# Optimization experiments

Hardware: AMD Instinct MI355X
Metric: run time of the kernel (lower is better)

The kernel has to match this reference:

```python
import jax, jax.numpy as jnp
import numpy as np

N = 100000      # number of nodes
FT = 256        # ft_in (hidden units)
NB_CLASSES = 16 # nb_classes
EPS = 1e-8      # torch.cosine_similarity eps


def setup_inputs() -> dict:
    key = jax.random.key(0)
    ks = jax.random.split(key, 7)
    seq = jax.random.normal(ks[0], (N, FT), dtype=jnp.float32)
    seq1 = jax.random.normal(ks[1], (N, FT), dtype=jnp.float32)
    labels = jax.random.randint(ks[2], (N,), 0, NB_CLASSES, dtype=jnp.int32)
    prompt1 = jax.random.normal(ks[3], (1, FT), dtype=jnp.float32)
    prompt2 = jax.random.normal(ks[4], (1, FT), dtype=jnp.float32)
    prompt3 = jax.random.normal(ks[5], (1, FT), dtype=jnp.float32)
    # weighted_prompt.reset_parameters: fixed init 0.5, 0.4, 0.3
    w_wp = jnp.array([[0.5, 0.4, 0.3]], dtype=jnp.float32)
    # weighted_feature.reset_parameters: fixed init 0.0, 1.0
    w_wf = jnp.array([[0.0, 1.0]], dtype=jnp.float32)
    # downstreamprompt.weight: xavier_uniform on [1, ft_in]
    bound = float(np.sqrt(6.0 / (1 + FT)))
    w_dp = jax.random.uniform(ks[6], (1, FT), jnp.float32, -bound, bound)
    a4 = jnp.array([0.1], dtype=jnp.float32)
    return {"seq": seq, "seq1": seq1, "labels": labels,
            "prompt1": prompt1, "prompt2": prompt2, "prompt3": prompt3,
            "w_wp": w_wp, "w_wf": w_wf, "w_dp": w_dp, "a4": a4}


def reference(seq, seq1, labels, prompt1, prompt2, prompt3, w_wp, w_wf, w_dp, a4):
    # weight = 1 + ELU(weighted_prompt(prompt))  -> [1, FT]
    prompt = jnp.concatenate([prompt1, prompt2, prompt3], axis=0)  # [3, FT]
    weight = 1.0 + jax.nn.elu(w_wp @ prompt)                       # [1, FT]
    rawret1 = weight * seq                                          # [N, FT]
    rawret2 = w_dp * seq                                            # downstreamprompt
    rawret3 = jax.nn.elu(w_wf[0, 0] * rawret1 + w_wf[0, 1] * rawret2)
    rawret = rawret3 + a4[0] * seq1                                 # [N, FT]
    # averageemb (train=1 path): per-class mean, zero-count classes stay 0
    sums = jax.ops.segment_sum(rawret, labels, num_segments=NB_CLASSES)  # [C, FT]
    counts = jax.ops.segment_sum(jnp.ones((rawret.shape[0],), rawret.dtype),
                                 labels, num_segments=NB_CLASSES)        # [C]
    ave = jnp.where(counts[:, None] > 0, sums / jnp.maximum(counts, 1.0)[:, None], sums)
    # fused per-pair cosine similarity: normalize + matmul (replaces N*C loop)
    num = rawret @ ave.T                                             # [N, C]
    denom = (jnp.linalg.norm(rawret, axis=1)[:, None] *
             jnp.linalg.norm(ave, axis=1)[None, :])
    ret = num / jnp.maximum(denom, EPS)
    return jax.nn.softmax(ret, axis=1)
```

## Files before the change

### kernel.cpp

```cpp
#include <hip/hip_runtime.h>
#include <hip/hip_bf16.h>

#define NROWS 100000
#define FT 256
#define NC 16
#define NBLK 512
#define NSL 8
#define SLICE (NBLK / NSL)

#define FPSCALE 1048576.0f
#define FPINV   (1.0f / 1048576.0f)

#define CW_AVEB 0
#define CW_NRM  2048
#define CW_PCNT 2064
#define CW_ST2C (CW_PCNT + NBLK*NC)
#define CW_ST2  (CW_ST2C + NSL*NC)
#define CW_PART (CW_ST2 + NSL*NC*FT)
#define CW_RAWB (CW_PART + NBLK*NC*FT)
#define CW_TOTAL (CW_RAWB + (NROWS*FT)/2)
#define CACHED_NEED_BYTES ((size_t)CW_TOTAL * 4)

#define WS_COEF 0
#define WS_SUMS 256
#define WS_CNTS 4352
#define WS_AVEB 4368
#define WS_NRM  6416

typedef float f32x4 __attribute__((ext_vector_type(4)));
typedef short bf16x8 __attribute__((ext_vector_type(8)));

static __device__ __forceinline__ float bfbits2f(unsigned int u16) {
    union { unsigned int i; float f; } v; v.i = u16 << 16; return v.f;
}
static __device__ __forceinline__ unsigned short f2bf(float f) {
    union { float f; unsigned int i; } v; v.f = f;
    unsigned int u = v.i;
    u += 0x7fffu + ((u >> 16) & 1u);
    return (unsigned short)(u >> 16);
}


__global__ __launch_bounds__(256) void k_accum_c(
    const float* __restrict__ seq,
    const float* __restrict__ seq1,
    const int* __restrict__ labels,
    const float* __restrict__ p1,
    const float* __restrict__ p2,
    const float* __restrict__ p3,
    const float* __restrict__ wwp,
    const float* __restrict__ wwf,
    const float* __restrict__ wdp,
    const float* __restrict__ a4p,
    float* __restrict__ ws)
{
    __shared__ __align__(16) float scoef[FT];
    __shared__ __align__(16) float lsumf[NC * FT];
    __shared__ int lcnti[4 * NC];
    const int tid = threadIdx.x;

    {
        float z = wwp[0] * p1[tid] + wwp[1] * p2[tid] + wwp[2] * p3[tid];
        float w = (z > 0.f) ? (1.f + z) : __expf(z);
        scoef[tid] = wwf[0] * w + wwf[1] * wdp[tid];
    }
    __syncthreads();

    const int wv = tid >> 6;
    const int l  = tid & 63;
    const int fl = l * 4;

    float cof[4];
    {
        const float4 c4 = *(const float4*)(scoef + fl);
        cof[0] = c4.x; cof[1] = c4.y; cof[2] = c4.z; cof[3] = c4.w;
    }
    const float a4v = a4p[0];
    unsigned int* rawb = (unsigned int*)(ws + CW_RAWB);

    float acc[NC][4];
#pragma unroll
    for (int c = 0; c < NC; ++c)
#pragma unroll
        for (int i = 0; i < 4; ++i) acc[c][i] = 0.f;
    int scnt[NC];
#pragma unroll
    for (int c = 0; c < NC; ++c) scnt[c] = 0;

    const int wg = blockIdx.x * 4 + wv;
    const int NQ = NROWS / 4;
    for (int q = wg; q < NQ; q += NBLK * 4) {
        const int r0 = q * 4;
        int lb[4]; float4 s4[4], t4[4];
#pragma unroll
        for (int j = 0; j < 4; ++j) {
            lb[j] = labels[r0 + j];
            s4[j] = *(const float4*)(seq  + (r0 + j) * FT + fl);
            t4[j] = *(const float4*)(seq1 + (r0 + j) * FT + fl);
        }
#pragma unroll
        for (int j = 0; j < 4; ++j) {
            const float ss[4] = {s4[j].x, s4[j].y, s4[j].z, s4[j].w};
            const float tt[4] = {t4[j].x, t4[j].y, t4[j].z, t4[j].w};
            float v[4];
#pragma unroll
            for (int i = 0; i < 4; ++i) {
                float u = cof[i] * ss[i];
                float r = (u > 0.f) ? u : (__expf(u) - 1.f);
                v[i] = r + a4v * tt[i];
            }
            uint2 pk;
            pk.x = (unsigned int)f2bf(v[0]) | ((unsigned int)f2bf(v[1]) << 16);
            pk.y = (unsigned int)f2bf(v[2]) | ((unsigned int)f2bf(v[3]) << 16);
            *(uint2*)(rawb + ((r0 + j) * FT + fl) / 2) = pk;
            const int ls = __builtin_amdgcn_readfirstlane(lb[j]);
#pragma unroll
            for (int c = 0; c < NC; ++c) {
                const float m = (ls == c) ? 1.0f : 0.0f;
#pragma unroll
                for (int i = 0; i < 4; ++i)
                    acc[c][i] = fmaf(m, v[i], acc[c][i]);
                scnt[c] += (ls == c) ? 1 : 0;
            }
        }
    }

    if (l == 0) {
#pragma unroll
        for (int c = 0; c < NC; ++c) lcnti[wv * NC + c] = scnt[c];
    }

    for (int w = 0; w < 4; ++w) {
        if (wv == w) {
#pragma unroll
            for (int c = 0; c < NC; ++c) {
                float4* p = (float4*)(lsumf + c * FT + fl);
                if (w == 0) {
                    float4 nv; nv.x = acc[c][0]; nv.y = acc[c][1];
                    nv.z = acc[c][2]; nv.w = acc[c][3];
                    *p = nv;
                } else {
                    float4 old = *p;
                    old.x += acc[c][0]; old.y += acc[c][1];
                    old.z += acc[c][2]; old.w += acc[c][3];
                    *p = old;
                }
            }
        }
        __syncthreads();
    }

    int* gpart = (int*)(ws + CW_PART) + blockIdx.x * (NC * FT);
    for (int idx = tid; idx < NC * FT; idx += 256)
        gpart[idx] = __float2int_rn(lsumf[idx] * FPSCALE);
    if (tid < NC) {
        int cc = lcnti[tid] + lcnti[NC + tid] + lcnti[2 * NC + tid]
               + lcnti[3 * NC + tid];
        ((int*)(ws + CW_PCNT))[blockIdx.x * NC + tid] = cc;
    }
}

__global__ __launch_bounds__(256) void k_reduce1(float* __restrict__ ws)
{
    const int c = blockIdx.x >> 3;
    const int r = blockIdx.x & 7;
    const int f = threadIdx.x;
    const int p0 = r * SLICE;
    const int* gpart = (const int*)(ws + CW_PART);
    int acc = 0;
#pragma unroll
    for (int p = 0; p < SLICE; ++p)
        acc += gpart[(p0 + p) * (NC * FT) + c * FT + f];
    ((int*)(ws + CW_ST2))[(r * NC + c) * FT + f] = acc;

    if (f < SLICE) {
        int cc = ((const int*)(ws + CW_PCNT))[(p0 + f) * NC + c];
#pragma unroll
        for (int o = 32; o > 0; o >>= 1) cc += __shfl_down(cc, o, 64);
        if (f == 0) ((int*)(ws + CW_ST2C))[r * NC + c] = cc;
    }
}

__global__ __launch_bounds__(256) void k_reduce2(float* __restrict__ ws)
{
    __shared__ float red[256];
    const int c = blockIdx.x;
    const int f = threadIdx.x;
    const int* st2  = (const int*)(ws + CW_ST2);
    const int* st2c = (const int*)(ws + CW_ST2C);
    long long isum = 0;
    int cnt = 0;
#pragma unroll
    for (int s = 0; s < NSL; ++s) {
        isum += (long long)st2[(s * NC + c) * FT + f];
        cnt  += st2c[s * NC + c];
    }
    float a = ((float)isum * FPINV) / fmaxf((float)cnt, 1.f);
    unsigned short ab = f2bf(a);
    ((unsigned short*)(ws + CW_AVEB))[c * FT + f] = ab;
    float af = bfbits2f(ab);

    red[f] = af * af;
    __syncthreads();
#pragma unroll
    for (int s = 128; s > 0; s >>= 1) {
        if (f < s) red[f] += red[f + s];
        __syncthreads();
    }
    if (f == 0) ws[CW_NRM + c] = sqrtf(red[0]);
}

__global__ __launch_bounds__(256) void k_out_c(
    const float* __restrict__ ws,
    float* __restrict__ out)
{
    const int tid = threadIdx.x;
    const int lane = tid & 63;
    const int wv   = tid >> 6;
    const int c = lane & 15;
    const int g = lane >> 4;

    const unsigned short* aveb = (const unsigned short*)(ws + CW_AVEB);
    const unsigned short* rawb = (const unsigned short*)(ws + CW_RAWB);
    bf16x8 bfrag[8];
#pragma unroll
    for (int kc = 0; kc < 8; ++kc)
        bfrag[kc] = *(const bf16x8*)(aveb + c * FT + kc * 32 + g * 8);
    const float na = ws[CW_NRM + c];

    const int ntiles = NROWS / 16;
    for (int tile = blockIdx.x * 4 + wv; tile < ntiles; tile += gridDim.x * 4) {
        const int rowbase = tile * 16;
        const int arow = rowbase + c;
        f32x4 accC = {0.f, 0.f, 0.f, 0.f};
        f32x4 accS = {0.f, 0.f, 0.f, 0.f};
#pragma unroll
        for (int kc = 0; kc < 8; ++kc) {
            bf16x8 afrag = *(const bf16x8*)(rawb + arow * FT + kc * 32 + g * 8);
            accC = __builtin_amdgcn_mfma_f32_16x16x32_bf16(afrag, bfrag[kc], accC, 0, 0, 0);
            accS = __builtin_amdgcn_mfma_f32_16x16x32_bf16(afrag, afrag,     accS, 0, 0, 0);
        }
#pragma unroll
        for (int q = 0; q < 4; ++q) {
            const float sd = __shfl(accS[q], g * 20 + q, 64);
            const float nr = sqrtf(fmaxf(sd, 0.f));
            const float denom = fmaxf(nr * na, 1e-8f);
            float cosv = accC[q] / denom;
            float mx = cosv;
#pragma unroll
            for (int o = 1; o < 16; o <<= 1) mx = fmaxf(mx, __shfl_xor(mx, o, 16));
            const float e = __expf(cosv - mx);
            float s = e;
#pragma unroll
            for (int o = 1; o < 16; o <<= 1) s += __shfl_xor(s, o, 16);
            out[(rowbase + g * 4 + q) * NC + c] = e / s;
        }
    }
}


__global__ void k_prep(const float* __restrict__ p1,
                       const float* __restrict__ p2,
                       const float* __restrict__ p3,
                       const float* __restrict__ wwp,
                       const float* __restrict__ wwf,
                       const float* __restrict__ wdp,
                       float* __restrict__ ws)
{
    int f = threadIdx.x;
    float z = wwp[0] * p1[f] + wwp[1] * p2[f] + wwp[2] * p3[f];
    float weight = (z > 0.f) ? (1.f + z) : __expf(z);
    ws[WS_COEF + f] = wwf[0] * weight + wwf[1] * wdp[f];
}

__global__ __launch_bounds__(1024) void k_accum(
    const float* __restrict__ seq,
    const float* __restrict__ seq1,
    const int* __restrict__ labels,
    const float* __restrict__ a4p,
    float* __restrict__ ws)
{
    __shared__ int lsum[NC * FT];
    __shared__ int lcnt[NC];
    const int tid = threadIdx.x;
    for (int i = tid; i < NC * FT; i += 1024) lsum[i] = 0;
    if (tid < NC) lcnt[tid] = 0;
    __syncthreads();

    const int rr = tid >> 5;
    const int m  = tid & 31;
    const int f0 = m * 8;
    const int mh = m >> 2;
    int off[8];
#pragma unroll
    for (int i = 0; i < 8; ++i) off[i] = (i + mh) & 7;

    float cof[8];
    {
        const float4 c0 = *(const float4*)(ws + WS_COEF + f0);
        const float4 c1 = *(const float4*)(ws + WS_COEF + f0 + 4);
        cof[0]=c0.x; cof[1]=c0.y; cof[2]=c0.z; cof[3]=c0.w;
        cof[4]=c1.x; cof[5]=c1.y; cof[6]=c1.z; cof[7]=c1.w;
    }
    const float a4v = a4p[0];

    for (int row = blockIdx.x * 32 + rr; row < NROWS; row += gridDim.x * 32) {
        const int lab = labels[row];
        const float4 sa  = *(const float4*)(seq  + row * FT + f0);
        const float4 sb  = *(const float4*)(seq  + row * FT + f0 + 4);
        const float4 ta  = *(const float4*)(seq1 + row * FT + f0);
        const float4 tb  = *(const float4*)(seq1 + row * FT + f0 + 4);
        const float s[8]  = {sa.x,sa.y,sa.z,sa.w, sb.x,sb.y,sb.z,sb.w};
        const float t[8]  = {ta.x,ta.y,ta.z,ta.w, tb.x,tb.y,tb.z,tb.w};
        int* base = lsum + lab * FT + f0;
#pragma unroll
        for (int i = 0; i < 8; ++i) {
            float u = cof[i] * s[i];
            float r = (u > 0.f) ? u : (__expf(u) - 1.f);
            atomicAdd(base + off[i], __float2int_rn((r + a4v * t[i]) * FPSCALE));
        }
        if (m == 0) atomicAdd(&lcnt[lab], 1);
    }
    __syncthreads();

    int* gsum = (int*)(ws + WS_SUMS);
    for (int idx = tid; idx < NC * FT; idx += 1024) {
        int p  = idx & 255;
        int mm = p >> 3;
        int r  = p & 7;
        int f  = (p & ~7) | ((r - (mm >> 2)) & 7);
        atomicAdd(gsum + (idx & ~255) + f, lsum[idx]);
    }
    if (tid < NC) atomicAdd((int*)(ws + WS_CNTS) + tid, lcnt[tid]);
}

__global__ void k_final(float* __restrict__ ws)
{
    __shared__ float nacc[NC];
    const int f = threadIdx.x;
    if (f < NC) nacc[f] = 0.f;
    __syncthreads();
    const int* gsum = (const int*)(ws + WS_SUMS);
    const int* gcnt = (const int*)(ws + WS_CNTS);
    unsigned short* aveb = (unsigned short*)(ws + WS_AVEB);
#pragma unroll
    for (int c = 0; c < NC; ++c) {
        float cnt = (float)gcnt[c];
        float a = ((float)gsum[c * FT + f] * FPINV) / fmaxf(cnt, 1.f);
        unsigned short ab = f2bf(a);
        aveb[c * FT + f] = ab;
        float af = bfbits2f(ab);
        atomicAdd(&nacc[c], af * af);
    }
    __syncthreads();
    if (f < NC) ws[WS_NRM + f] = sqrtf(nacc[f]);
}

__global__ __launch_bounds__(256) void k_out(
    const float* __restrict__ seq,
    const float* __restrict__ seq1,
    const float* __restrict__ a4p,
    const float* __restrict__ ws,
    float* __restrict__ out)
{
    __shared__ __align__(16) float scoef[FT];
    const int tid = threadIdx.x;
    for (int i = tid; i < FT; i += 256) scoef[i] = ws[WS_COEF + i];
    __syncthreads();

    const int lane = tid & 63;
    const int wv   = tid >> 6;
    const int c = lane & 15;
    const int g = lane >> 4;

    const unsigned short* aveb = (const unsigned short*)(ws + WS_AVEB);
    bf16x8 bfrag[8];
#pragma unroll
    for (int kc = 0; kc < 8; ++kc)
        bfrag[kc] = *(const bf16x8*)(aveb + c * FT + kc * 32 + g * 8);
    const float na  = ws[WS_NRM + c];
    const float a4v = a4p[0];

    const int ntiles = NROWS / 16;
    for (int tile = blockIdx.x * 4 + wv; tile < ntiles; tile += gridDim.x * 4) {
        const int rowbase = tile * 16;
        const int arow = rowbase + c;
        f32x4 accC = {0.f, 0.f, 0.f, 0.f};
        f32x4 accS = {0.f, 0.f, 0.f, 0.f};
#pragma unroll
        for (int kc = 0; kc < 8; ++kc) {
            const int k0 = kc * 32 + g * 8;
            const float4 sa = *(const float4*)(seq  + arow * FT + k0);
            const float4 sb = *(const float4*)(seq  + arow * FT + k0 + 4);
            const float4 ta = *(const float4*)(seq1 + arow * FT + k0);
            const float4 tb = *(const float4*)(seq1 + arow * FT + k0 + 4);
            const float4 c0 = *(const float4*)(scoef + k0);
            const float4 c1 = *(const float4*)(scoef + k0 + 4);
            const float s[8]  = {sa.x,sa.y,sa.z,sa.w, sb.x,sb.y,sb.z,sb.w};
            const float t[8]  = {ta.x,ta.y,ta.z,ta.w, tb.x,tb.y,tb.z,tb.w};
            const float cf[8] = {c0.x,c0.y,c0.z,c0.w, c1.x,c1.y,c1.z,c1.w};
            bf16x8 afrag;
#pragma unroll
            for (int i = 0; i < 8; ++i) {
                float u = cf[i] * s[i];
                float r = (u > 0.f) ? u : (__expf(u) - 1.f);
                afrag[i] = (short)f2bf(r + a4v * t[i]);
            }
            accC = __builtin_amdgcn_mfma_f32_16x16x32_bf16(afrag, bfrag[kc], accC, 0, 0, 0);
            accS = __builtin_amdgcn_mfma_f32_16x16x32_bf16(afrag, afrag,     accS, 0, 0, 0);
        }
#pragma unroll
        for (int q = 0; q < 4; ++q) {
            const float sd = __shfl(accS[q], g * 20 + q, 64);
            const float nr = sqrtf(fmaxf(sd, 0.f));
            const float denom = fmaxf(nr * na, 1e-8f);
            float cosv = accC[q] / denom;
            float mx = cosv;
#pragma unroll
            for (int o = 1; o < 16; o <<= 1) mx = fmaxf(mx, __shfl_xor(mx, o, 16));
            const float e = __expf(cosv - mx);
            float s = e;
#pragma unroll
            for (int o = 1; o < 16; o <<= 1) s += __shfl_xor(s, o, 16);
            out[(rowbase + g * 4 + q) * NC + c] = e / s;
        }
    }
}

extern "C" void kernel_launch(void* const* d_in, const int* in_sizes, int n_in,
                              void* d_out, int out_size, void* d_ws, size_t ws_size,
                              hipStream_t stream)
{
    const float* seq  = (const float*)d_in[0];
    const float* seq1 = (const float*)d_in[1];
    const int*   lab  = (const int*)d_in[2];
    const float* p1   = (const float*)d_in[3];
    const float* p2   = (const float*)d_in[4];
    const float* p3   = (const float*)d_in[5];
    const float* wwp  = (const float*)d_in[6];
    const float* wwf  = (const float*)d_in[7];
    const float* wdp  = (const float*)d_in[8];
    const float* a4   = (const float*)d_in[9];
    float* ws  = (float*)d_ws;
    float* out = (float*)d_out;

    if (ws_size >= CACHED_NEED_BYTES) {
        k_accum_c<<<NBLK,     256, 0, stream>>>(seq, seq1, lab, p1, p2, p3,
                                                wwp, wwf, wdp, a4, ws);
        k_reduce1<<<NC * NSL, 256, 0, stream>>>(ws);
        k_reduce2<<<NC,       256, 0, stream>>>(ws);
        k_out_c  <<<1568,     256, 0, stream>>>(ws, out);
    } else {
        hipMemsetAsync((char*)d_ws + WS_SUMS * sizeof(int), 0,
                       (NC * FT + NC) * sizeof(int), stream);
        k_prep <<<1,    256, 0, stream>>>(p1, p2, p3, wwp, wwf, wdp, ws);
        k_accum<<<512, 1024, 0, stream>>>(seq, seq1, lab, a4, ws);
        k_final<<<1,    256, 0, stream>>>(ws);
        k_out  <<<1568, 256, 0, stream>>>(seq, seq1, a4, ws, out);
    }
}
```

Measured before the change: 267.9 us.

## Widen accumulation kernel to 1024 threads with half-row wave split

```diff
diff --git a/kernel.cpp b/kernel.cpp
--- a/kernel.cpp
+++ b/kernel.cpp
@@ -41,7 +41,7 @@
 }
 
 
-__global__ __launch_bounds__(256) void k_accum_c(
+__global__ __launch_bounds__(1024, 8) void k_accum_c(
     const float* __restrict__ seq,
     const float* __restrict__ seq1,
     const int* __restrict__ labels,
@@ -56,10 +56,10 @@
 {
     __shared__ __align__(16) float scoef[FT];
     __shared__ __align__(16) float lsumf[NC * FT];
-    __shared__ int lcnti[4 * NC];
+    __shared__ int lcnti[16 * NC];
     const int tid = threadIdx.x;
 
-    {
+    if (tid < FT) {
         float z = wwp[0] * p1[tid] + wwp[1] * p2[tid] + wwp[2] * p3[tid];
         float w = (z > 0.f) ? (1.f + z) : __expf(z);
         scoef[tid] = wwf[0] * w + wwf[1] * wdp[tid];
@@ -68,82 +68,95 @@
 
     const int wv = tid >> 6;
     const int l  = tid & 63;
-    const int fl = l * 4;
-
-    float cof[4];
+    const int h  = wv & 1;
+    const int rbase = blockIdx.x * 8 + (wv >> 1);
+    const int fb = h * 128 + l * 2;
+
+    float2 cof2;
     {
-        const float4 c4 = *(const float4*)(scoef + fl);
-        cof[0] = c4.x; cof[1] = c4.y; cof[2] = c4.z; cof[3] = c4.w;
+        cof2 = *(const float2*)(scoef + fb);
     }
     const float a4v = a4p[0];
     unsigned int* rawb = (unsigned int*)(ws + CW_RAWB);
 
-    float acc[NC][4];
-#pragma unroll
-    for (int c = 0; c < NC; ++c)
-#pragma unroll
-        for (int i = 0; i < 4; ++i) acc[c][i] = 0.f;
-    int scnt[NC];
-#pragma unroll
-    for (int c = 0; c < NC; ++c) scnt[c] = 0;
-
-    const int wg = blockIdx.x * 4 + wv;
-    const int NQ = NROWS / 4;
-    for (int q = wg; q < NQ; q += NBLK * 4) {
-        const int r0 = q * 4;
-        int lb[4]; float4 s4[4], t4[4];
-#pragma unroll
-        for (int j = 0; j < 4; ++j) {
-            lb[j] = labels[r0 + j];
-            s4[j] = *(const float4*)(seq  + (r0 + j) * FT + fl);
-            t4[j] = *(const float4*)(seq1 + (r0 + j) * FT + fl);
-        }
-#pragma unroll
-        for (int j = 0; j < 4; ++j) {
-            const float ss[4] = {s4[j].x, s4[j].y, s4[j].z, s4[j].w};
-            const float tt[4] = {t4[j].x, t4[j].y, t4[j].z, t4[j].w};
-            float v[4];
-#pragma unroll
-            for (int i = 0; i < 4; ++i) {
-                float u = cof[i] * ss[i];
-                float r = (u > 0.f) ? u : (__expf(u) - 1.f);
-                v[i] = r + a4v * tt[i];
+    float acc[NC][2];
+#pragma unroll
+    for (int c = 0; c < NC; ++c) { acc[c][0] = 0.f; acc[c][1] = 0.f; }
+    unsigned int scnt4[4] = {0u, 0u, 0u, 0u};
+
+    for (int r = rbase; r < NROWS; r += 8192) {
+        const int rA = r;
+        const int rB2 = r + 4096;
+        const bool vB = rB2 < NROWS;
+        const int rB = vB ? rB2 : rA;
+        const int lA = labels[rA];
+        const int lB = labels[rB];
+        const float2 sA = *(const float2*)(seq  + rA * FT + fb);
+        const float2 tA = *(const float2*)(seq1 + rA * FT + fb);
+        const float2 sB = *(const float2*)(seq  + rB * FT + fb);
+        const float2 tB = *(const float2*)(seq1 + rB * FT + fb);
+
+        float vA0, vA1;
+        {
+            float u0 = cof2.x * sA.x;
+            float e0 = (u0 > 0.f) ? u0 : (__expf(u0) - 1.f);
+            vA0 = e0 + a4v * tA.x;
+            float u1 = cof2.y * sA.y;
+            float e1 = (u1 > 0.f) ? u1 : (__expf(u1) - 1.f);
+            vA1 = e1 + a4v * tA.y;
+        }
+        rawb[(rA * FT + fb) >> 1] =
+            (unsigned int)f2bf(vA0) | ((unsigned int)f2bf(vA1) << 16);
+        const int lsA = __builtin_amdgcn_readfirstlane(lA);
+#pragma unroll
+        for (int c = 0; c < NC; ++c) {
+            const float m = (lsA == c) ? 1.0f : 0.0f;
+            acc[c][0] = fmaf(m, vA0, acc[c][0]);
+            acc[c][1] = fmaf(m, vA1, acc[c][1]);
+            scnt4[c >> 2] += (lsA == c) ? (1u << (8 * (c & 3))) : 0u;
+        }
+
+        float vB0, vB1;
+        {
+            float u0 = cof2.x * sB.x;
+            float e0 = (u0 > 0.f) ? u0 : (__expf(u0) - 1.f);
+            vB0 = e0 + a4v * tB.x;
+            float u1 = cof2.y * sB.y;
+            float e1 = (u1 > 0.f) ? u1 : (__expf(u1) - 1.f);
+            vB1 = e1 + a4v * tB.y;
+        }
+        const int lsB = __builtin_amdgcn_readfirstlane(lB);
+        if (vB) {
+            rawb[(rB * FT + fb) >> 1] =
+                (unsigned int)f2bf(vB0) | ((unsigned int)f2bf(vB1) << 16);
+#pragma unroll
+            for (int c = 0; c < NC; ++c) {
+                const float m = (lsB == c) ? 1.0f : 0.0f;
+                acc[c][0] = fmaf(m, vB0, acc[c][0]);
+                acc[c][1] = fmaf(m, vB1, acc[c][1]);
+                scnt4[c >> 2] += (lsB == c) ? (1u << (8 * (c & 3))) : 0u;
             }
-            uint2 pk;
-            pk.x = (unsigned int)f2bf(v[0]) | ((unsigned int)f2bf(v[1]) << 16);
-            pk.y = (unsigned int)f2bf(v[2]) | ((unsigned int)f2bf(v[3]) << 16);
-            *(uint2*)(rawb + ((r0 + j) * FT + fl) / 2) = pk;
-            const int ls = __builtin_amdgcn_readfirstlane(lb[j]);
+        }
+    }
+
+    if (l == 0) {
+#pragma unroll
+        for (int c = 0; c < NC; ++c)
+            lcnti[wv * NC + c] = (int)((scnt4[c >> 2] >> (8 * (c & 3))) & 255u);
+    }
+
+    for (int w = 0; w < 16; ++w) {
+        if (wv == w) {
 #pragma unroll
             for (int c = 0; c < NC; ++c) {
-                const float m = (ls == c) ? 1.0f : 0.0f;
-#pragma unroll
-                for (int i = 0; i < 4; ++i)
-                    acc[c][i] = fmaf(m, v[i], acc[c][i]);
-                scnt[c] += (ls == c) ? 1 : 0;
-            }
-        }
-    }
-
-    if (l == 0) {
-#pragma unroll
-        for (int c = 0; c < NC; ++c) lcnti[wv * NC + c] = scnt[c];
-    }
-
-    for (int w = 0; w < 4; ++w) {
-        if (wv == w) {
-#pragma unroll
-            for (int c = 0; c < NC; ++c) {
-                float4* p = (float4*)(lsumf + c * FT + fl);
-                if (w == 0) {
-                    float4 nv; nv.x = acc[c][0]; nv.y = acc[c][1];
-                    nv.z = acc[c][2]; nv.w = acc[c][3];
+                float2* p = (float2*)(lsumf + c * FT + fb);
+                if (w < 2) {
+                    float2 nv; nv.x = acc[c][0]; nv.y = acc[c][1];
                     *p = nv;
                 } else {
-                    float4 old = *p;
-                    old.x += acc[c][0]; old.y += acc[c][1];
-                    old.z += acc[c][2]; old.w += acc[c][3];
-                    *p = old;
+                    float2 o = *p;
+                    o.x += acc[c][0]; o.y += acc[c][1];
+                    *p = o;
                 }
             }
         }
@@ -151,11 +164,12 @@
     }
 
     int* gpart = (int*)(ws + CW_PART) + blockIdx.x * (NC * FT);
-    for (int idx = tid; idx < NC * FT; idx += 256)
+    for (int idx = tid; idx < NC * FT; idx += 1024)
         gpart[idx] = __float2int_rn(lsumf[idx] * FPSCALE);
     if (tid < NC) {
-        int cc = lcnti[tid] + lcnti[NC + tid] + lcnti[2 * NC + tid]
-               + lcnti[3 * NC + tid];
+        int cc = 0;
+#pragma unroll
+        for (int w = 0; w < 16; w += 2) cc += lcnti[w * NC + tid];
         ((int*)(ws + CW_PCNT))[blockIdx.x * NC + tid] = cc;
     }
 }
@@ -445,7 +459,7 @@
     float* out = (float*)d_out;
 
     if (ws_size >= CACHED_NEED_BYTES) {
-        k_accum_c<<<NBLK,     256, 0, stream>>>(seq, seq1, lab, p1, p2, p3,
+        k_accum_c<<<NBLK,    1024, 0, stream>>>(seq, seq1, lab, p1, p2, p3,
                                                 wwp, wwf, wdp, a4, ws);
         k_reduce1<<<NC * NSL, 256, 0, stream>>>(ws);
         k_reduce2<<<NC,       256, 0, stream>>>(ws);
```

After: 271.4 us. No clear change (+1.3%).

## Fuse accumulate, reduce and output stages into one cooperative kernel with grid syncs

Applied to the files above, without the earlier changes.

```diff
diff --git a/kernel.cpp b/kernel.cpp
--- a/kernel.cpp
+++ b/kernel.cpp
@@ -1,5 +1,8 @@
 #include <hip/hip_runtime.h>
 #include <hip/hip_bf16.h>
+#include <hip/hip_cooperative_groups.h>
+
+namespace cg = cooperative_groups;
 
 #define NROWS 100000
 #define FT 256
@@ -38,6 +41,231 @@
     unsigned int u = v.i;
     u += 0x7fffu + ((u >> 16) & 1u);
     return (unsigned short)(u >> 16);
+}
+
+__global__ __launch_bounds__(256, 2) void k_fused(
+    const float* __restrict__ seq,
+    const float* __restrict__ seq1,
+    const int* __restrict__ labels,
+    const float* __restrict__ p1,
+    const float* __restrict__ p2,
+    const float* __restrict__ p3,
+    const float* __restrict__ wwp,
+    const float* __restrict__ wwf,
+    const float* __restrict__ wdp,
+    const float* __restrict__ a4p,
+    float* __restrict__ ws,
+    float* __restrict__ out)
+{
+    cg::grid_group grid = cg::this_grid();
+    __shared__ __align__(16) float scoef[FT];
+    __shared__ __align__(16) float lsumf[NC * FT];
+    __shared__ int lcnti[4 * NC];
+    __shared__ float red[256];
+    const int tid = threadIdx.x;
+    const int bid = blockIdx.x;
+
+    {
+        float z = wwp[0] * p1[tid] + wwp[1] * p2[tid] + wwp[2] * p3[tid];
+        float w = (z > 0.f) ? (1.f + z) : __expf(z);
+        scoef[tid] = wwf[0] * w + wwf[1] * wdp[tid];
+    }
+    __syncthreads();
+
+    {
+        const int wv = tid >> 6;
+        const int l  = tid & 63;
+        const int fl = l * 4;
+
+        float cof[4];
+        {
+            const float4 c4 = *(const float4*)(scoef + fl);
+            cof[0] = c4.x; cof[1] = c4.y; cof[2] = c4.z; cof[3] = c4.w;
+        }
+        const float a4v = a4p[0];
+        unsigned int* rawb = (unsigned int*)(ws + CW_RAWB);
+
+        float acc[NC][4];
+#pragma unroll
+        for (int c = 0; c < NC; ++c)
+#pragma unroll
+            for (int i = 0; i < 4; ++i) acc[c][i] = 0.f;
+        int scnt[NC];
+#pragma unroll
+        for (int c = 0; c < NC; ++c) scnt[c] = 0;
+
+        const int wg = bid * 4 + wv;
+        const int NQ = NROWS / 4;
+        for (int q = wg; q < NQ; q += NBLK * 4) {
+            const int r0 = q * 4;
+            int lb[4]; float4 s4[4], t4[4];
+#pragma unroll
+            for (int j = 0; j < 4; ++j) {
+                lb[j] = labels[r0 + j];
+                s4[j] = *(const float4*)(seq  + (r0 + j) * FT + fl);
+                t4[j] = *(const float4*)(seq1 + (r0 + j) * FT + fl);
+            }
+#pragma unroll
+            for (int j = 0; j < 4; ++j) {
+                const float ss[4] = {s4[j].x, s4[j].y, s4[j].z, s4[j].w};
+                const float tt[4] = {t4[j].x, t4[j].y, t4[j].z, t4[j].w};
+                float v[4];
+#pragma unroll
+                for (int i = 0; i < 4; ++i) {
+                    float u = cof[i] * ss[i];
+                    float r = (u > 0.f) ? u : (__expf(u) - 1.f);
+                    v[i] = r + a4v * tt[i];
+                }
+                uint2 pk;
+                pk.x = (unsigned int)f2bf(v[0]) | ((unsigned int)f2bf(v[1]) << 16);
+                pk.y = (unsigned int)f2bf(v[2]) | ((unsigned int)f2bf(v[3]) << 16);
+                *(uint2*)(rawb + ((r0 + j) * FT + fl) / 2) = pk;
+                const int ls = __builtin_amdgcn_readfirstlane(lb[j]);
+#pragma unroll
+                for (int c = 0; c < NC; ++c) {
+                    const float m = (ls == c) ? 1.0f : 0.0f;
+#pragma unroll
+                    for (int i = 0; i < 4; ++i)
+                        acc[c][i] = fmaf(m, v[i], acc[c][i]);
+                    scnt[c] += (ls == c) ? 1 : 0;
+                }
+            }
+        }
+
+        if (l == 0) {
+#pragma unroll
+            for (int c = 0; c < NC; ++c) lcnti[wv * NC + c] = scnt[c];
+        }
+
+        for (int w = 0; w < 4; ++w) {
+            if (wv == w) {
+#pragma unroll
+                for (int c = 0; c < NC; ++c) {
+                    float4* p = (float4*)(lsumf + c * FT + fl);
+                    if (w == 0) {
+                        float4 nv; nv.x = acc[c][0]; nv.y = acc[c][1];
+                        nv.z = acc[c][2]; nv.w = acc[c][3];
+                        *p = nv;
+                    } else {
+                        float4 old = *p;
+                        old.x += acc[c][0]; old.y += acc[c][1];
+                        old.z += acc[c][2]; old.w += acc[c][3];
+                        *p = old;
+                    }
+                }
+            }
+            __syncthreads();
+        }
+
+        int* gpart = (int*)(ws + CW_PART) + bid * (NC * FT);
+        for (int idx = tid; idx < NC * FT; idx += 256)
+            __builtin_nontemporal_store(__float2int_rn(lsumf[idx] * FPSCALE),
+                                        gpart + idx);
+        if (tid < NC) {
+            int cc = lcnti[tid] + lcnti[NC + tid] + lcnti[2 * NC + tid]
+                   + lcnti[3 * NC + tid];
+            __builtin_nontemporal_store(cc,
+                (int*)(ws + CW_PCNT) + bid * NC + tid);
+        }
+    }
+
+    grid.sync();
+
+    if (bid < NC * NSL) {
+        const int c = bid >> 3;
+        const int r = bid & 7;
+        const int f = tid;
+        const int p0 = r * SLICE;
+        const int* gpart = (const int*)(ws + CW_PART);
+        int acc = 0;
+#pragma unroll
+        for (int p = 0; p < SLICE; ++p)
+            acc += __builtin_nontemporal_load(
+                gpart + (p0 + p) * (NC * FT) + c * FT + f);
+        ((int*)(ws + CW_ST2))[(r * NC + c) * FT + f] = acc;
+
+        if (f < SLICE) {
+            int cc = ((const int*)(ws + CW_PCNT))[(p0 + f) * NC + c];
+#pragma unroll
+            for (int o = 32; o > 0; o >>= 1) cc += __shfl_down(cc, o, 64);
+            if (f == 0) ((int*)(ws + CW_ST2C))[r * NC + c] = cc;
+        }
+    }
+
+    grid.sync();
+
+    if (bid < NC) {
+        const int c = bid;
+        const int f = tid;
+        const int* st2  = (const int*)(ws + CW_ST2);
+        const int* st2c = (const int*)(ws + CW_ST2C);
+        long long isum = 0;
+        int cnt = 0;
+#pragma unroll
+        for (int s = 0; s < NSL; ++s) {
+            isum += (long long)st2[(s * NC + c) * FT + f];
+            cnt  += st2c[s * NC + c];
+        }
+        float a = ((float)isum * FPINV) / fmaxf((float)cnt, 1.f);
+        unsigned short ab = f2bf(a);
+        ((unsigned short*)(ws + CW_AVEB))[c * FT + f] = ab;
+        float af = bfbits2f(ab);
+
+        red[f] = af * af;
+        __syncthreads();
+#pragma unroll
+        for (int s = 128; s > 0; s >>= 1) {
+            if (f < s) red[f] += red[f + s];
+            __syncthreads();
+        }
+        if (f == 0) ws[CW_NRM + c] = sqrtf(red[0]);
+    }
+
+    grid.sync();
+
+    {
+        const int lane = tid & 63;
+        const int wv   = tid >> 6;
+        const int c = lane & 15;
+        const int g = lane >> 4;
+
+        const unsigned short* aveb = (const unsigned short*)(ws + CW_AVEB);
+        const unsigned short* rawb = (const unsigned short*)(ws + CW_RAWB);
+        bf16x8 bfrag[8];
+#pragma unroll
+        for (int kc = 0; kc < 8; ++kc)
+            bfrag[kc] = *(const bf16x8*)(aveb + c * FT + kc * 32 + g * 8);
+        const float na = ws[CW_NRM + c];
+
+        const int ntiles = NROWS / 16;
+        for (int tile = bid * 4 + wv; tile < ntiles; tile += NBLK * 4) {
+            const int rowbase = tile * 16;
+            const int arow = rowbase + c;
+            f32x4 accC = {0.f, 0.f, 0.f, 0.f};
+            f32x4 accS = {0.f, 0.f, 0.f, 0.f};
+#pragma unroll
+            for (int kc = 0; kc < 8; ++kc) {
+                bf16x8 afrag = *(const bf16x8*)(rawb + arow * FT + kc * 32 + g * 8);
+                accC = __builtin_amdgcn_mfma_f32_16x16x32_bf16(afrag, bfrag[kc], accC, 0, 0, 0);
+                accS = __builtin_amdgcn_mfma_f32_16x16x32_bf16(afrag, afrag,     accS, 0, 0, 0);
+            }
+#pragma unroll
+            for (int q = 0; q < 4; ++q) {
+                const float sd = __shfl(accS[q], g * 20 + q, 64);
+                const float nr = sqrtf(fmaxf(sd, 0.f));
+                const float denom = fmaxf(nr * na, 1e-8f);
+                float cosv = accC[q] / denom;
+                float mx = cosv;
+#pragma unroll
+                for (int o = 1; o < 16; o <<= 1) mx = fmaxf(mx, __shfl_xor(mx, o, 16));
+                const float e = __expf(cosv - mx);
+                float s = e;
+#pragma unroll
+                for (int o = 1; o < 16; o <<= 1) s += __shfl_xor(s, o, 16);
+                out[(rowbase + g * 4 + q) * NC + c] = e / s;
+            }
+        }
+    }
 }
 
 
@@ -152,11 +380,13 @@
 
     int* gpart = (int*)(ws + CW_PART) + blockIdx.x * (NC * FT);
     for (int idx = tid; idx < NC * FT; idx += 256)
-        gpart[idx] = __float2int_rn(lsumf[idx] * FPSCALE);
+        __builtin_nontemporal_store(__float2int_rn(lsumf[idx] * FPSCALE),
+                                    gpart + idx);
     if (tid < NC) {
         int cc = lcnti[tid] + lcnti[NC + tid] + lcnti[2 * NC + tid]
                + lcnti[3 * NC + tid];
-        ((int*)(ws + CW_PCNT))[blockIdx.x * NC + tid] = cc;
+        __builtin_nontemporal_store(cc,
+            (int*)(ws + CW_PCNT) + blockIdx.x * NC + tid);
     }
 }
 
@@ -170,7 +400,8 @@
     int acc = 0;
 #pragma unroll
     for (int p = 0; p < SLICE; ++p)
-        acc += gpart[(p0 + p) * (NC * FT) + c * FT + f];
+        acc += __builtin_nontemporal_load(
+            gpart + (p0 + p) * (NC * FT) + c * FT + f);
     ((int*)(ws + CW_ST2))[(r * NC + c) * FT + f] = acc;
 
     if (f < SLICE) {
@@ -445,11 +676,19 @@
     float* out = (float*)d_out;
 
     if (ws_size >= CACHED_NEED_BYTES) {
-        k_accum_c<<<NBLK,     256, 0, stream>>>(seq, seq1, lab, p1, p2, p3,
-                                                wwp, wwf, wdp, a4, ws);
-        k_reduce1<<<NC * NSL, 256, 0, stream>>>(ws);
-        k_reduce2<<<NC,       256, 0, stream>>>(ws);
-        k_out_c  <<<1568,     256, 0, stream>>>(ws, out);
+        void* args[] = {(void*)&seq, (void*)&seq1, (void*)&lab,
+                        (void*)&p1, (void*)&p2, (void*)&p3,
+                        (void*)&wwp, (void*)&wwf, (void*)&wdp, (void*)&a4,
+                        (void*)&ws, (void*)&out};
+        hipError_t e = hipLaunchCooperativeKernel(
+            (const void*)k_fused, dim3(NBLK), dim3(256), args, 0, stream);
+        if (e != hipSuccess) {
+            k_accum_c<<<NBLK,     256, 0, stream>>>(seq, seq1, lab, p1, p2, p3,
+                                                    wwp, wwf, wdp, a4, ws);
+            k_reduce1<<<NC * NSL, 256, 0, stream>>>(ws);
+            k_reduce2<<<NC,       256, 0, stream>>>(ws);
+            k_out_c  <<<1568,     256, 0, stream>>>(ws, out);
+        }
     } else {
         hipMemsetAsync((char*)d_ws + WS_SUMS * sizeof(int), 0,
                        (NC * FT + NC) * sizeof(int), stream);
```

Measured after the change: 459.4 us. 71.5% more time.
